# Optimization experiments

Hardware: AMD Instinct MI355X
Metric: run time of the kernel (lower is better)

Reference implementation:

```python
import jax, jax.numpy as jnp
import numpy as np

PRE_NMS = 4096
POST_NMS = 500
NMS_THRESH = 0.7


def setup_inputs() -> dict:
    key = jax.random.key(0)
    k1, k2, k3, k4, k5 = jax.random.split(key, 5)
    B, A = 4, 500000
    # anchors: [x, y, z, w, l, h, ry] with positive sizes, realistic ranges
    ctr = jax.random.uniform(k1, (B, A, 3)) * jnp.array([80.0, 80.0, 4.0])
    size = 1.0 + jax.random.uniform(k2, (B, A, 3)) * 3.0
    ry = (jax.random.uniform(k3, (B, A, 1)) - 0.5) * np.pi
    anchors = jnp.concatenate([ctr, size, ry], axis=-1)
    objectness = jax.random.normal(k4, (B, A))
    box_regression = jax.random.normal(k5, (B, A, 7)) * 0.1
    return {"anchors": anchors, "objectness": objectness, "box_regression": box_regression}


def decode(rel, anc):
    # SECOND-style 3D box decode (BoxCoder.decode)
    xa, ya, za = anc[..., 0], anc[..., 1], anc[..., 2]
    wa, la, ha = anc[..., 3], anc[..., 4], anc[..., 5]
    ra = anc[..., 6]
    diag = jnp.sqrt(wa * wa + la * la)
    xg = rel[..., 0] * diag + xa
    yg = rel[..., 1] * diag + ya
    zg = rel[..., 2] * ha + za
    wg = jnp.exp(rel[..., 3]) * wa
    lg = jnp.exp(rel[..., 4]) * la
    hg = jnp.exp(rel[..., 5]) * ha
    rg = rel[..., 6] + ra
    return jnp.stack([xg, yg, zg, wg, lg, hg, rg], axis=-1)


def bev_iou(b):
    # pairwise axis-aligned bird's-eye-view IoU; b: [K,7]
    x, y, w, l = b[:, 0], b[:, 1], b[:, 3], b[:, 4]
    x1, x2 = x - w * 0.5, x + w * 0.5
    y1, y2 = y - l * 0.5, y + l * 0.5
    iw = jnp.clip(jnp.minimum(x2[:, None], x2[None, :]) - jnp.maximum(x1[:, None], x1[None, :]), 0.0)
    ih = jnp.clip(jnp.minimum(y2[:, None], y2[None, :]) - jnp.maximum(y1[:, None], y1[None, :]), 0.0)
    inter = iw * ih
    area = w * l
    return inter / (area[:, None] + area[None, :] - inter + 1e-6)


def nms_keep(iou, thresh):
    # greedy NMS over score-sorted candidates; returns bool keep mask [K]
    K = iou.shape[0]
    idx = jnp.arange(K)

    def body(i, keep):
        sup = keep[i] & (iou[i] > thresh) & (idx > i)
        return keep & ~sup

    return jax.lax.fori_loop(0, K, body, jnp.ones((K,), dtype=bool))


def _per_image(anc, obj, reg):
    scores = jax.nn.sigmoid(obj)                    # [A]
    s_top, topk_idx = jax.lax.top_k(scores, PRE_NMS)  # sorted desc
    boxes = decode(reg[topk_idx], anc[topk_idx])      # [K,7]
    keep = nms_keep(bev_iou(boxes), NMS_THRESH)
    masked = jnp.where(keep, s_top, -1.0)
    _, sel = jax.lax.top_k(masked, POST_NMS)          # top post_nms kept boxes
    out_boxes = boxes[sel]                            # [P,7]
    out_scores = s_top[sel]                           # [P]
    return jnp.concatenate([out_boxes, out_scores[:, None]], axis=-1)  # [P,8]


def reference(anchors, objectness, box_regression):
    return jax.vmap(_per_image)(anchors, objectness, box_regression)  # [B,P,8]
```

## Files before the change

### kernel.cpp

```cpp
#include <hip/hip_runtime.h>
#include <hip/hip_bf16.h>

#define B_IMG 4
#define PRE_NMS 4096
#define POST_NMS 500
#define CAND_CAP 8192
#define BND_CAP 65536

typedef unsigned long long ull;

__device__ __forceinline__ unsigned key_of(float f) {
    unsigned u = __float_as_uint(f);
    return (u & 0x80000000u) ? ~u : (u | 0x80000000u);
}

__global__ void init_kernel(uint2* state, unsigned* hist, unsigned* count) {
    int t = blockIdx.x * blockDim.x + threadIdx.x;
    if (t < B_IMG) state[t] = make_uint2(0u, (unsigned)PRE_NMS);
    if (t < 2 * B_IMG) count[t] = 0u;
    if (t < B_IMG * 256) hist[t] = 0u;
}

__global__ void hist0_kernel(const float* __restrict__ obj, unsigned* __restrict__ hist, int A) {
    int b = blockIdx.y;
    __shared__ unsigned h[256];
    int t = threadIdx.x;
    int lane = t & 63;
    if (t < 256) h[t] = 0u;
    __syncthreads();
    const float* o = obj + (size_t)b * A;
    int stride = gridDim.x * blockDim.x;
    for (int i = blockIdx.x * blockDim.x + t;; i += stride) {
        bool valid = (i < A);
        ull vm = __ballot(valid);
        if (!vm) break;
        unsigned bin = valid ? (key_of(o[i]) >> 24) : 0xFFFFFFFFu;
        ull active = vm;
        while (active) {
            int leader = __ffsll((long long)active) - 1;
            unsigned lb = __shfl(bin, leader);
            ull m = __ballot(bin == lb) & active;
            if (lane == leader) atomicAdd(&h[lb], (unsigned)__popcll(m));
            active &= ~m;
        }
    }
    __syncthreads();
    if (t < 256 && h[t]) atomicAdd(&hist[b * 256 + t], h[t]);
}

__global__ void scan0_kernel(uint2* state, const unsigned* __restrict__ hist) {
    int b = threadIdx.x;
    if (b < B_IMG) {
        const unsigned* h = hist + b * 256;
        unsigned kneed = state[b].y;
        unsigned cum = 0;
        int d;
        for (d = 255; d > 0; d--) {
            unsigned c = h[d];
            if (cum + c >= kneed) break;
            cum += c;
        }
        state[b].x = (unsigned)d;
        state[b].y = kneed - cum;
    }
}

__global__ void compact_kernel(const float* __restrict__ obj, const uint2* __restrict__ state,
                               ull* __restrict__ bnd, unsigned* __restrict__ count, int A) {
    int b = blockIdx.y;
    unsigned d0 = state[b].x;
    __shared__ ull buf[2048];
    __shared__ unsigned lcnt, base;
    int t = threadIdx.x;
    if (t == 0) lcnt = 0u;
    __syncthreads();
    const float* o = obj + (size_t)b * A;
    int stride = gridDim.x * blockDim.x;
    for (int i = blockIdx.x * blockDim.x + t; i < A; i += stride) {
        unsigned key = key_of(o[i]);
        if ((key >> 24) >= d0) {
            unsigned p = atomicAdd(&lcnt, 1u);
            if (p < 2048u)
                buf[p] = ((ull)key << 32) | (unsigned)(0xFFFFFFFFu - (unsigned)i);
        }
    }
    __syncthreads();
    unsigned c = lcnt < 2048u ? lcnt : 2048u;
    if (t == 0) base = atomicAdd(&count[B_IMG + b], c);
    __syncthreads();
    for (unsigned p = t; p < c; p += blockDim.x) {
        unsigned pos = base + p;
        if (pos < BND_CAP) bnd[(size_t)b * BND_CAP + pos] = buf[p];
    }
}

__global__ void __launch_bounds__(1024) refine_kernel(const ull* __restrict__ bnd,
                                                      uint2* state,
                                                      ull* __restrict__ cand,
                                                      unsigned* __restrict__ count) {
    int b = blockIdx.x;
    __shared__ unsigned h[256];
    __shared__ unsigned sh_prefix, sh_kneed, sh_pos;
    int t = threadIdx.x;
    unsigned n = count[B_IMG + b];
    if (n > BND_CAP) n = BND_CAP;
    const ull* L = bnd + (size_t)b * BND_CAP;
    if (t == 0) { sh_prefix = state[b].x; sh_kneed = state[b].y; sh_pos = 0u; }
    for (int pass = 1; pass < 4; pass++) {
        if (t < 256) h[t] = 0u;
        __syncthreads();
        unsigned prefix = sh_prefix;
        int sh = 32 - 8 * pass;
        int dsh = 24 - 8 * pass;
        for (unsigned i = t; i < n; i += 1024) {
            unsigned key = (unsigned)(L[i] >> 32);
            if ((key >> sh) == prefix) atomicAdd(&h[(key >> dsh) & 255u], 1u);
        }
        __syncthreads();
        if (t == 0) {
            unsigned kneed = sh_kneed, cum = 0;
            int d;
            for (d = 255; d > 0; d--) {
                unsigned c = h[d];
                if (cum + c >= kneed) break;
                cum += c;
            }
            sh_prefix = (prefix << 8) | (unsigned)d;
            sh_kneed = kneed - cum;
        }
        __syncthreads();
    }
    unsigned T = sh_prefix;
    for (unsigned i = t; i < n; i += 1024) {
        ull v = L[i];
        if ((unsigned)(v >> 32) >= T) {
            unsigned p = atomicAdd(&sh_pos, 1u);
            if (p < CAND_CAP) cand[(size_t)b * CAND_CAP + p] = v;
        }
    }
    __syncthreads();
    if (t == 0) count[b] = sh_pos < CAND_CAP ? sh_pos : CAND_CAP;
}

__global__ void __launch_bounds__(256) rank_kernel(const ull* __restrict__ cand,
                                                   const unsigned* __restrict__ count,
                                                   unsigned* __restrict__ topk_idx,
                                                   const float* __restrict__ obj,
                                                   float* __restrict__ s_top, int A) {
    __shared__ ull s[CAND_CAP];
    int b = blockIdx.y;
    int t = threadIdx.x;
    unsigned cnt = count[b];
    if (cnt > CAND_CAP) cnt = CAND_CAP;
    const ull* C = cand + (size_t)b * CAND_CAP;
    unsigned cntR = (cnt + 7u) & ~7u;
    for (unsigned i = t; i < cntR; i += 256) s[i] = (i < cnt) ? C[i] : 0ull;
    __syncthreads();
    unsigned c = blockIdx.x * 256 + t;
    if (c >= cnt) return;
    ull me = s[c];
    unsigned rank = 0;
#pragma unroll 1
    for (unsigned j = 0; j < cntR; j += 8) {
        rank += (unsigned)(s[j]     > me) + (unsigned)(s[j + 1] > me)
              + (unsigned)(s[j + 2] > me) + (unsigned)(s[j + 3] > me)
              + (unsigned)(s[j + 4] > me) + (unsigned)(s[j + 5] > me)
              + (unsigned)(s[j + 6] > me) + (unsigned)(s[j + 7] > me);
    }
    if (rank < PRE_NMS) {
        unsigned idx = 0xFFFFFFFFu - (unsigned)(me & 0xFFFFFFFFull);
        topk_idx[b * PRE_NMS + rank] = idx;
        float x = obj[(size_t)b * A + idx];
        s_top[b * PRE_NMS + rank] = 1.0f / (1.0f + expf(-x));
    }
}

__global__ void decode_kernel(const float* __restrict__ anchors, const float* __restrict__ reg,
                              const unsigned* __restrict__ topk_idx, float* __restrict__ boxes,
                              float* __restrict__ X1, float* __restrict__ X2,
                              float* __restrict__ Y1, float* __restrict__ Y2,
                              float* __restrict__ AREA, int A) {
    int b = blockIdx.y;
    int r = blockIdx.x * 256 + threadIdx.x;
    if (r >= PRE_NMS) return;
    unsigned idx = topk_idx[b * PRE_NMS + r];
    const float* an = anchors + ((size_t)b * A + idx) * 7;
    const float* rg = reg + ((size_t)b * A + idx) * 7;
    float xa = an[0], ya = an[1], za = an[2], wa = an[3], la = an[4], ha = an[5], ra = an[6];
    float diag = sqrtf(wa * wa + la * la);
    float xg = rg[0] * diag + xa;
    float yg = rg[1] * diag + ya;
    float zg = rg[2] * ha + za;
    float wg = expf(rg[3]) * wa;
    float lg = expf(rg[4]) * la;
    float hg = expf(rg[5]) * ha;
    float rr = rg[6] + ra;
    float* o = boxes + ((size_t)b * PRE_NMS + r) * 7;
    o[0] = xg; o[1] = yg; o[2] = zg; o[3] = wg; o[4] = lg; o[5] = hg; o[6] = rr;
    int q = b * PRE_NMS + r;
    X1[q] = xg - wg * 0.5f;
    X2[q] = xg + wg * 0.5f;
    Y1[q] = yg - lg * 0.5f;
    Y2[q] = yg + lg * 0.5f;
    AREA[q] = wg * lg;
}

__global__ void mask_kernel(const float* __restrict__ X1, const float* __restrict__ X2,
                            const float* __restrict__ Y1, const float* __restrict__ Y2,
                            const float* __restrict__ AREA, ull* __restrict__ mask) {
    int b = blockIdx.y;
    int t = blockIdx.x * 256 + threadIdx.x;
    int i = t & (PRE_NMS - 1);
    int w = t >> 12;
    int q0 = b * PRE_NMS;
    float x1i = X1[q0 + i], x2i = X2[q0 + i];
    float y1i = Y1[q0 + i], y2i = Y2[q0 + i];
    float ai = AREA[q0 + i];
    ull word = 0ull;
    int jbase = w << 6;
#pragma unroll 4
    for (int k = 0; k < 64; k++) {
        int j = jbase + k;
        float iw = fminf(x2i, X2[q0 + j]) - fmaxf(x1i, X1[q0 + j]);
        iw = fmaxf(iw, 0.0f);
        float ih = fminf(y2i, Y2[q0 + j]) - fmaxf(y1i, Y1[q0 + j]);
        ih = fmaxf(ih, 0.0f);
        float inter = iw * ih;
        float den = ai + AREA[q0 + j] - inter + 1e-6f;
        float iou = inter / den;
        word |= ((ull)((iou > 0.7f) && (j > i))) << k;
    }
    mask[((size_t)b * PRE_NMS + i) * 64 + w] = word;
}

#define LOAD_TILE(BUF, WT) do {                                               \
    const ull* _base = Mb + ((size_t)(WT) << 12) + lane;                      \
    _Pragma("unroll")                                                         \
    for (int _k = 0; _k < 64; _k++) BUF[_k] = _base[(size_t)_k << 6];         \
} while (0)

#define LOAD_D(DST, WT) (DST) = Mb[((size_t)(WT) << 12) + ((size_t)lane << 6) + (WT)]

#define PROCESS(W, CURB, DCUR, NXTB, DNXT) do {                               \
    ull cur = __shfl(K, (W));                                                 \
    if ((W) + 1 < 64) { LOAD_D(DNXT, (W) + 1); LOAD_TILE(NXTB, (W) + 1); }    \
    ull active = __ballot((DCUR) != 0ull) & cur;                              \
    while (active) {                                                          \
        int _kk = __ffsll((long long)active) - 1;                             \
        ull dk = __shfl((DCUR), _kk);                                         \
        cur &= ~dk; active &= ~dk; active &= ~(1ull << _kk);                  \
    }                                                                         \
    ull sup = 0ull;                                                           \
    _Pragma("unroll")                                                         \
    for (int _k = 0; _k < 64; _k++)                                           \
        sup |= ((cur >> _k) & 1ull) ? CURB[_k] : 0ull;                        \
    K &= ~sup;                                                                \
} while (0)

__global__ void __launch_bounds__(64, 1) nms_kernel(const ull* __restrict__ mask,
                                                    ull* __restrict__ keep_out) {
    int b = blockIdx.x;
    int lane = threadIdx.x;
    const ull* Mb = mask + (size_t)b * PRE_NMS * 64;
    ull K = ~0ull;
    ull bufA[64], bufB[64];
    ull da = 0ull, db = 0ull;
    LOAD_D(da, 0);
    LOAD_TILE(bufA, 0);
    for (int w = 0; w < 64; w += 2) {
        PROCESS(w, bufA, da, bufB, db);
        PROCESS(w + 1, bufB, db, bufA, da);
    }
    keep_out[b * 64 + lane] = K;
}

__global__ void select_write_kernel(const ull* __restrict__ keep,
                                    const float* __restrict__ boxes,
                                    const float* __restrict__ s_top,
                                    float* __restrict__ out) {
    int b = blockIdx.x;
    __shared__ int cnts[64];
    __shared__ int bases[65];
    __shared__ int sel[POST_NMS];
    int t = threadIdx.x;
    if (t < 64) cnts[t] = __popcll(keep[b * 64 + t]);
    __syncthreads();
    if (t == 0) {
        int acc = 0;
        for (int w = 0; w < 64; w++) { bases[w] = acc; acc += cnts[w]; }
        bases[64] = acc;
    }
    __syncthreads();
    if (t < 64) {
        ull kw = keep[b * 64 + t];
        int K_total = bases[64];
        int kr = bases[t];
        int ur = t * 64 - bases[t];
        for (int k = 0; k < 64; k++) {
            int i = t * 64 + k;
            if ((kw >> k) & 1ull) {
                if (kr < POST_NMS) sel[kr] = i;
                kr++;
            } else {
                int pos = K_total + ur;
                if (pos < POST_NMS) sel[pos] = i;
                ur++;
            }
        }
    }
    __syncthreads();
    for (int r = t; r < POST_NMS; r += 512) {
        int i = sel[r];
        const float* bx = boxes + ((size_t)b * PRE_NMS + i) * 7;
        float* o = out + ((size_t)b * POST_NMS + r) * 8;
#pragma unroll
        for (int c = 0; c < 7; c++) o[c] = bx[c];
        o[7] = s_top[b * PRE_NMS + i];
    }
}

extern "C" void kernel_launch(void* const* d_in, const int* in_sizes, int n_in,
                              void* d_out, int out_size, void* d_ws, size_t ws_size,
                              hipStream_t stream) {
    const float* anchors = (const float*)d_in[0];
    const float* obj = (const float*)d_in[1];
    const float* reg = (const float*)d_in[2];
    float* out = (float*)d_out;
    const int A = in_sizes[1] / B_IMG;

    auto align = [](size_t x) { return (x + 255) & ~(size_t)255; };
    char* p = (char*)d_ws;
    uint2* state = (uint2*)p;     p += align(B_IMG * sizeof(uint2));
    unsigned* hist = (unsigned*)p; p += align(B_IMG * 256 * sizeof(unsigned));
    unsigned* count = (unsigned*)p; p += align(2 * B_IMG * sizeof(unsigned));
    ull* cand = (ull*)p;          p += align((size_t)B_IMG * CAND_CAP * 8);
    ull* bnd = (ull*)p;           p += align((size_t)B_IMG * BND_CAP * 8);
    unsigned* topk = (unsigned*)p; p += align((size_t)B_IMG * PRE_NMS * 4);
    float* s_top = (float*)p;     p += align((size_t)B_IMG * PRE_NMS * 4);
    float* boxes = (float*)p;     p += align((size_t)B_IMG * PRE_NMS * 7 * 4);
    float* X1 = (float*)p;        p += align((size_t)B_IMG * PRE_NMS * 4);
    float* X2 = (float*)p;        p += align((size_t)B_IMG * PRE_NMS * 4);
    float* Y1 = (float*)p;        p += align((size_t)B_IMG * PRE_NMS * 4);
    float* Y2 = (float*)p;        p += align((size_t)B_IMG * PRE_NMS * 4);
    float* AREA = (float*)p;      p += align((size_t)B_IMG * PRE_NMS * 4);
    ull* mask = (ull*)p;          p += align((size_t)B_IMG * PRE_NMS * 64 * 8);
    ull* keep = (ull*)p;          p += align((size_t)B_IMG * 64 * 8);

    init_kernel<<<4, 256, 0, stream>>>(state, hist, count);
    hist0_kernel<<<dim3(256, B_IMG), 256, 0, stream>>>(obj, hist, A);
    scan0_kernel<<<1, 64, 0, stream>>>(state, hist);
    compact_kernel<<<dim3(256, B_IMG), 256, 0, stream>>>(obj, state, bnd, count, A);
    refine_kernel<<<B_IMG, 1024, 0, stream>>>(bnd, state, cand, count);
    rank_kernel<<<dim3(CAND_CAP / 256, B_IMG), 256, 0, stream>>>(cand, count, topk, obj, s_top, A);
    decode_kernel<<<dim3(PRE_NMS / 256, B_IMG), 256, 0, stream>>>(anchors, reg, topk, boxes,
                                                                  X1, X2, Y1, Y2, AREA, A);
    mask_kernel<<<dim3(PRE_NMS * 64 / 256, B_IMG), 256, 0, stream>>>(X1, X2, Y1, Y2, AREA, mask);
    nms_kernel<<<B_IMG, 64, 0, stream>>>(mask, keep);
    select_write_kernel<<<B_IMG, 512, 0, stream>>>(keep, boxes, s_top, out);
}
```

Before: 390.8 us.

## Fuse rank/decode and NMS/select kernels, vectorize histogram and compaction

Replaces the ballot-based histogram with float4 loads into four replicated shared histograms and writes per-block partial histograms, so the init kernel and global atomics go away. The scan kernel now also resets the counters. Compaction reads float4. Rank and decode are fused into one kernel that reads candidates straight from global memory and recovers the score from the key. The mask kernel writes zeros for tiles whose mask can only be zero, the NMS scan is spread across 4 wavefronts with shared-memory reductions, and it is fused with the select/write step. Together these cut launches and memory traffic, at the cost of more barriers inside the NMS loop.

Result: slower. 460.3 us (+17.8%).

```diff
diff --git a/kernel.cpp b/kernel.cpp
--- a/kernel.cpp
+++ b/kernel.cpp
@@ -6,6 +6,7 @@
 #define POST_NMS 500
 #define CAND_CAP 8192
 #define BND_CAP 65536
+#define HBLK 256
 
 typedef unsigned long long ull;
 
@@ -14,54 +15,52 @@
     return (u & 0x80000000u) ? ~u : (u | 0x80000000u);
 }
 
-__global__ void init_kernel(uint2* state, unsigned* hist, unsigned* count) {
-    int t = blockIdx.x * blockDim.x + threadIdx.x;
-    if (t < B_IMG) state[t] = make_uint2(0u, (unsigned)PRE_NMS);
-    if (t < 2 * B_IMG) count[t] = 0u;
-    if (t < B_IMG * 256) hist[t] = 0u;
-}
-
-__global__ void hist0_kernel(const float* __restrict__ obj, unsigned* __restrict__ hist, int A) {
+__global__ void hist0_kernel(const float* __restrict__ obj, unsigned* __restrict__ histPart, int A) {
     int b = blockIdx.y;
+    __shared__ unsigned h[4][256];
+    int t = threadIdx.x;
+#pragma unroll
+    for (int r = 0; r < 4; r++) h[r][t] = 0u;
+    __syncthreads();
+    const float4* o4 = (const float4*)(obj + (size_t)b * A);
+    int n4 = A >> 2;
+    int stride = gridDim.x * blockDim.x;
+    int rep = t & 3;
+    for (int i = blockIdx.x * blockDim.x + t; i < n4; i += stride) {
+        float4 v = o4[i];
+        atomicAdd(&h[rep][key_of(v.x) >> 24], 1u);
+        atomicAdd(&h[rep][key_of(v.y) >> 24], 1u);
+        atomicAdd(&h[rep][key_of(v.z) >> 24], 1u);
+        atomicAdd(&h[rep][key_of(v.w) >> 24], 1u);
+    }
+    if (blockIdx.x == 0 && t < (A & 3)) {
+        unsigned k = key_of(obj[(size_t)b * A + (A & ~3) + t]);
+        atomicAdd(&h[rep][k >> 24], 1u);
+    }
+    __syncthreads();
+    histPart[((size_t)b * HBLK + blockIdx.x) * 256 + t] = h[0][t] + h[1][t] + h[2][t] + h[3][t];
+}
+
+__global__ void scan0_kernel(uint2* state, const unsigned* __restrict__ histPart,
+                             unsigned* __restrict__ count) {
+    int b = blockIdx.x;
+    int t = threadIdx.x;
     __shared__ unsigned h[256];
-    int t = threadIdx.x;
-    int lane = t & 63;
-    if (t < 256) h[t] = 0u;
-    __syncthreads();
-    const float* o = obj + (size_t)b * A;
-    int stride = gridDim.x * blockDim.x;
-    for (int i = blockIdx.x * blockDim.x + t;; i += stride) {
-        bool valid = (i < A);
-        ull vm = __ballot(valid);
-        if (!vm) break;
-        unsigned bin = valid ? (key_of(o[i]) >> 24) : 0xFFFFFFFFu;
-        ull active = vm;
-        while (active) {
-            int leader = __ffsll((long long)active) - 1;
-            unsigned lb = __shfl(bin, leader);
-            ull m = __ballot(bin == lb) & active;
-            if (lane == leader) atomicAdd(&h[lb], (unsigned)__popcll(m));
-            active &= ~m;
-        }
-    }
-    __syncthreads();
-    if (t < 256 && h[t]) atomicAdd(&hist[b * 256 + t], h[t]);
-}
-
-__global__ void scan0_kernel(uint2* state, const unsigned* __restrict__ hist) {
-    int b = threadIdx.x;
-    if (b < B_IMG) {
-        const unsigned* h = hist + b * 256;
-        unsigned kneed = state[b].y;
-        unsigned cum = 0;
+    unsigned s = 0;
+    for (int blk = 0; blk < HBLK; blk++) s += histPart[((size_t)b * HBLK + blk) * 256 + t];
+    h[t] = s;
+    __syncthreads();
+    if (t == 0) {
+        unsigned kneed = PRE_NMS, cum = 0;
         int d;
         for (d = 255; d > 0; d--) {
             unsigned c = h[d];
             if (cum + c >= kneed) break;
             cum += c;
         }
-        state[b].x = (unsigned)d;
-        state[b].y = kneed - cum;
+        state[b] = make_uint2((unsigned)d, kneed - cum);
+        count[b] = 0u;
+        count[B_IMG + b] = 0u;
     }
 }
 
@@ -74,15 +73,22 @@
     int t = threadIdx.x;
     if (t == 0) lcnt = 0u;
     __syncthreads();
-    const float* o = obj + (size_t)b * A;
+    const float4* o4 = (const float4*)(obj + (size_t)b * A);
+    int n4 = A >> 2;
     int stride = gridDim.x * blockDim.x;
-    for (int i = blockIdx.x * blockDim.x + t; i < A; i += stride) {
-        unsigned key = key_of(o[i]);
-        if ((key >> 24) >= d0) {
-            unsigned p = atomicAdd(&lcnt, 1u);
-            if (p < 2048u)
-                buf[p] = ((ull)key << 32) | (unsigned)(0xFFFFFFFFu - (unsigned)i);
-        }
+    for (int i = blockIdx.x * blockDim.x + t; i < n4; i += stride) {
+        float4 v = o4[i];
+        unsigned i0 = (unsigned)i * 4u;
+        unsigned k0 = key_of(v.x), k1 = key_of(v.y), k2 = key_of(v.z), k3 = key_of(v.w);
+        if ((k0 >> 24) >= d0) { unsigned p = atomicAdd(&lcnt, 1u); if (p < 2048u) buf[p] = ((ull)k0 << 32) | (0xFFFFFFFFu - i0); }
+        if ((k1 >> 24) >= d0) { unsigned p = atomicAdd(&lcnt, 1u); if (p < 2048u) buf[p] = ((ull)k1 << 32) | (0xFFFFFFFFu - (i0 + 1u)); }
+        if ((k2 >> 24) >= d0) { unsigned p = atomicAdd(&lcnt, 1u); if (p < 2048u) buf[p] = ((ull)k2 << 32) | (0xFFFFFFFFu - (i0 + 2u)); }
+        if ((k3 >> 24) >= d0) { unsigned p = atomicAdd(&lcnt, 1u); if (p < 2048u) buf[p] = ((ull)k3 << 32) | (0xFFFFFFFFu - (i0 + 3u)); }
+    }
+    if (blockIdx.x == 0 && t < (A & 3)) {
+        unsigned ii = (unsigned)(A & ~3) + t;
+        unsigned k = key_of(obj[(size_t)b * A + ii]);
+        if ((k >> 24) >= d0) { unsigned p = atomicAdd(&lcnt, 1u); if (p < 2048u) buf[p] = ((ull)k << 32) | (0xFFFFFFFFu - ii); }
     }
     __syncthreads();
     unsigned c = lcnt < 2048u ? lcnt : 2048u;
@@ -95,7 +101,7 @@
 }
 
 __global__ void __launch_bounds__(1024) refine_kernel(const ull* __restrict__ bnd,
-                                                      uint2* state,
+                                                      const uint2* __restrict__ state,
                                                       ull* __restrict__ cand,
                                                       unsigned* __restrict__ count) {
     int b = blockIdx.x;
@@ -110,8 +116,7 @@
         if (t < 256) h[t] = 0u;
         __syncthreads();
         unsigned prefix = sh_prefix;
-        int sh = 32 - 8 * pass;
-        int dsh = 24 - 8 * pass;
+        int sh = 32 - 8 * pass, dsh = 24 - 8 * pass;
         for (unsigned i = t; i < n; i += 1024) {
             unsigned key = (unsigned)(L[i] >> 32);
             if ((key >> sh) == prefix) atomicAdd(&h[(key >> dsh) & 255u], 1u);
@@ -135,69 +140,58 @@
         ull v = L[i];
         if ((unsigned)(v >> 32) >= T) {
             unsigned p = atomicAdd(&sh_pos, 1u);
-            if (p < CAND_CAP) cand[(size_t)b * CAND_CAP + p] = v;
-        }
-    }
-    __syncthreads();
-    if (t == 0) count[b] = sh_pos < CAND_CAP ? sh_pos : CAND_CAP;
-}
-
-__global__ void __launch_bounds__(256) rank_kernel(const ull* __restrict__ cand,
-                                                   const unsigned* __restrict__ count,
-                                                   unsigned* __restrict__ topk_idx,
-                                                   const float* __restrict__ obj,
-                                                   float* __restrict__ s_top, int A) {
-    __shared__ ull s[CAND_CAP];
+            if (p < CAND_CAP) cand[(size_t)b * (CAND_CAP + 8) + p] = v;
+        }
+    }
+    __syncthreads();
+    if (t < 8) {
+        unsigned cc = sh_pos < CAND_CAP ? sh_pos : CAND_CAP;
+        cand[(size_t)b * (CAND_CAP + 8) + cc + t] = 0ull;
+        if (t == 0) count[b] = cc;
+    }
+}
+
+__global__ void __launch_bounds__(256) rankdecode_kernel(
+        const ull* __restrict__ cand, const unsigned* __restrict__ count,
+        const float* __restrict__ anchors, const float* __restrict__ reg,
+        float* __restrict__ boxes, float* __restrict__ X1, float* __restrict__ X2,
+        float* __restrict__ Y1, float* __restrict__ Y2, float* __restrict__ AREA,
+        float* __restrict__ s_top, int A) {
     int b = blockIdx.y;
-    int t = threadIdx.x;
     unsigned cnt = count[b];
     if (cnt > CAND_CAP) cnt = CAND_CAP;
-    const ull* C = cand + (size_t)b * CAND_CAP;
+    unsigned c = blockIdx.x * 256 + threadIdx.x;
+    if (c >= cnt) return;
+    const ull* C = cand + (size_t)b * (CAND_CAP + 8);
+    ull me = C[c];
     unsigned cntR = (cnt + 7u) & ~7u;
-    for (unsigned i = t; i < cntR; i += 256) s[i] = (i < cnt) ? C[i] : 0ull;
-    __syncthreads();
-    unsigned c = blockIdx.x * 256 + t;
-    if (c >= cnt) return;
-    ull me = s[c];
     unsigned rank = 0;
-#pragma unroll 1
     for (unsigned j = 0; j < cntR; j += 8) {
-        rank += (unsigned)(s[j]     > me) + (unsigned)(s[j + 1] > me)
-              + (unsigned)(s[j + 2] > me) + (unsigned)(s[j + 3] > me)
-              + (unsigned)(s[j + 4] > me) + (unsigned)(s[j + 5] > me)
-              + (unsigned)(s[j + 6] > me) + (unsigned)(s[j + 7] > me);
-    }
-    if (rank < PRE_NMS) {
-        unsigned idx = 0xFFFFFFFFu - (unsigned)(me & 0xFFFFFFFFull);
-        topk_idx[b * PRE_NMS + rank] = idx;
-        float x = obj[(size_t)b * A + idx];
-        s_top[b * PRE_NMS + rank] = 1.0f / (1.0f + expf(-x));
-    }
-}
-
-__global__ void decode_kernel(const float* __restrict__ anchors, const float* __restrict__ reg,
-                              const unsigned* __restrict__ topk_idx, float* __restrict__ boxes,
-                              float* __restrict__ X1, float* __restrict__ X2,
-                              float* __restrict__ Y1, float* __restrict__ Y2,
-                              float* __restrict__ AREA, int A) {
-    int b = blockIdx.y;
-    int r = blockIdx.x * 256 + threadIdx.x;
-    if (r >= PRE_NMS) return;
-    unsigned idx = topk_idx[b * PRE_NMS + r];
+        rank += (unsigned)(C[j]     > me) + (unsigned)(C[j + 1] > me)
+              + (unsigned)(C[j + 2] > me) + (unsigned)(C[j + 3] > me)
+              + (unsigned)(C[j + 4] > me) + (unsigned)(C[j + 5] > me)
+              + (unsigned)(C[j + 6] > me) + (unsigned)(C[j + 7] > me);
+    }
+    if (rank >= PRE_NMS) return;
+    unsigned key = (unsigned)(me >> 32);
+    unsigned idx = 0xFFFFFFFFu - (unsigned)(me & 0xFFFFFFFFull);
+    unsigned ub = (key & 0x80000000u) ? (key & 0x7FFFFFFFu) : ~key;
+    float x = __uint_as_float(ub);
+    s_top[b * PRE_NMS + rank] = 1.0f / (1.0f + expf(-x));
     const float* an = anchors + ((size_t)b * A + idx) * 7;
     const float* rg = reg + ((size_t)b * A + idx) * 7;
     float xa = an[0], ya = an[1], za = an[2], wa = an[3], la = an[4], ha = an[5], ra = an[6];
-    float diag = sqrtf(wa * wa + la * la);
-    float xg = rg[0] * diag + xa;
-    float yg = rg[1] * diag + ya;
+    float diagv = sqrtf(wa * wa + la * la);
+    float xg = rg[0] * diagv + xa;
+    float yg = rg[1] * diagv + ya;
     float zg = rg[2] * ha + za;
     float wg = expf(rg[3]) * wa;
     float lg = expf(rg[4]) * la;
     float hg = expf(rg[5]) * ha;
     float rr = rg[6] + ra;
-    float* o = boxes + ((size_t)b * PRE_NMS + r) * 7;
+    float* o = boxes + ((size_t)b * PRE_NMS + rank) * 7;
     o[0] = xg; o[1] = yg; o[2] = zg; o[3] = wg; o[4] = lg; o[5] = hg; o[6] = rr;
-    int q = b * PRE_NMS + r;
+    int q = b * PRE_NMS + rank;
     X1[q] = xg - wg * 0.5f;
     X2[q] = xg + wg * 0.5f;
     Y1[q] = yg - lg * 0.5f;
@@ -212,6 +206,8 @@
     int t = blockIdx.x * 256 + threadIdx.x;
     int i = t & (PRE_NMS - 1);
     int w = t >> 12;
+    size_t mi = ((size_t)b * PRE_NMS + i) * 64 + w;
+    if (i >= ((w + 1) << 6)) { mask[mi] = 0ull; return; }
     int q0 = b * PRE_NMS;
     float x1i = X1[q0 + i], x2i = X2[q0 + i];
     float y1i = Y1[q0 + i], y2i = Y2[q0 + i];
@@ -230,60 +226,75 @@
         float iou = inter / den;
         word |= ((ull)((iou > 0.7f) && (j > i))) << k;
     }
-    mask[((size_t)b * PRE_NMS + i) * 64 + w] = word;
-}
-
-#define LOAD_TILE(BUF, WT) do {                                               \
-    const ull* _base = Mb + ((size_t)(WT) << 12) + lane;                      \
-    _Pragma("unroll")                                                         \
-    for (int _k = 0; _k < 64; _k++) BUF[_k] = _base[(size_t)_k << 6];         \
-} while (0)
-
-#define LOAD_D(DST, WT) (DST) = Mb[((size_t)(WT) << 12) + ((size_t)lane << 6) + (WT)]
-
-#define PROCESS(W, CURB, DCUR, NXTB, DNXT) do {                               \
-    ull cur = __shfl(K, (W));                                                 \
-    if ((W) + 1 < 64) { LOAD_D(DNXT, (W) + 1); LOAD_TILE(NXTB, (W) + 1); }    \
-    ull active = __ballot((DCUR) != 0ull) & cur;                              \
-    while (active) {                                                          \
-        int _kk = __ffsll((long long)active) - 1;                             \
-        ull dk = __shfl((DCUR), _kk);                                         \
-        cur &= ~dk; active &= ~dk; active &= ~(1ull << _kk);                  \
-    }                                                                         \
-    ull sup = 0ull;                                                           \
-    _Pragma("unroll")                                                         \
-    for (int _k = 0; _k < 64; _k++)                                           \
-        sup |= ((cur >> _k) & 1ull) ? CURB[_k] : 0ull;                        \
-    K &= ~sup;                                                                \
-} while (0)
-
-__global__ void __launch_bounds__(64, 1) nms_kernel(const ull* __restrict__ mask,
-                                                    ull* __restrict__ keep_out) {
+    mask[mi] = word;
+}
+
+__global__ void __launch_bounds__(256, 1) nms_select_kernel(
+        const ull* __restrict__ mask, const float* __restrict__ boxes,
+        const float* __restrict__ s_top, float* __restrict__ out) {
     int b = blockIdx.x;
-    int lane = threadIdx.x;
+    int t = threadIdx.x;
+    int lane = t & 63, v = t >> 6;
+    int rbase = v * 16;
     const ull* Mb = mask + (size_t)b * PRE_NMS * 64;
-    ull K = ~0ull;
-    ull bufA[64], bufB[64];
-    ull da = 0ull, db = 0ull;
-    LOAD_D(da, 0);
-    LOAD_TILE(bufA, 0);
-    for (int w = 0; w < 64; w += 2) {
-        PROCESS(w, bufA, da, bufB, db);
-        PROCESS(w + 1, bufB, db, bufA, da);
-    }
-    keep_out[b * 64 + lane] = K;
-}
-
-__global__ void select_write_kernel(const ull* __restrict__ keep,
-                                    const float* __restrict__ boxes,
-                                    const float* __restrict__ s_top,
-                                    float* __restrict__ out) {
-    int b = blockIdx.x;
+    __shared__ ull diag[2][64];
+    __shared__ ull part[2][4][64];
+    __shared__ ull keepw[64];
     __shared__ int cnts[64];
     __shared__ int bases[65];
     __shared__ int sel[POST_NMS];
-    int t = threadIdx.x;
-    if (t < 64) cnts[t] = __popcll(keep[b * 64 + t]);
+    ull K = ~0ull;
+    ull b0[16], b1[16], b2[16], b3[16];
+
+#define PREF(W, BUF) do {                                                          \
+    _Pragma("unroll")                                                              \
+    for (int kk = 0; kk < 16; kk++)                                                \
+        BUF[kk] = Mb[(((size_t)(W) * 64 + rbase + kk) << 6) + lane];               \
+} while (0)
+
+#define TILE(W, BUF) do {                                                          \
+    int par = (W) & 1;                                                             \
+    ull cur = __shfl(K, (W));                                                      \
+    if (lane == (W)) {                                                             \
+        _Pragma("unroll")                                                          \
+        for (int kk = 0; kk < 16; kk++) diag[par][rbase + kk] = BUF[kk];           \
+    }                                                                              \
+    __syncthreads();                                                               \
+    ull dl = diag[par][lane];                                                      \
+    ull active = __ballot(dl != 0ull) & cur;                                       \
+    while (active) {                                                               \
+        int kk = __ffsll((long long)active) - 1;                                   \
+        ull dk = __shfl(dl, kk);                                                   \
+        cur &= ~dk; active &= ~dk; active &= ~(1ull << kk);                        \
+    }                                                                              \
+    ull sup = 0ull;                                                                \
+    _Pragma("unroll")                                                              \
+    for (int kk = 0; kk < 16; kk++)                                                \
+        sup |= ((cur >> (rbase + kk)) & 1ull) ? BUF[kk] : 0ull;                    \
+    part[par][v][lane] = sup;                                                      \
+    __syncthreads();                                                               \
+    K &= ~(part[par][0][lane] | part[par][1][lane] |                               \
+           part[par][2][lane] | part[par][3][lane]);                               \
+    if ((W) + 4 < 64) {                                                            \
+        _Pragma("unroll")                                                          \
+        for (int kk = 0; kk < 16; kk++)                                            \
+            BUF[kk] = Mb[((((size_t)(W) + 4) * 64 + rbase + kk) << 6) + lane];     \
+    }                                                                              \
+} while (0)
+
+    PREF(0, b0); PREF(1, b1); PREF(2, b2); PREF(3, b3);
+    for (int w = 0; w < 64; w += 4) {
+        TILE(w + 0, b0);
+        TILE(w + 1, b1);
+        TILE(w + 2, b2);
+        TILE(w + 3, b3);
+    }
+#undef PREF
+#undef TILE
+
+    if (v == 0) keepw[lane] = K;
+    __syncthreads();
+    if (t < 64) cnts[t] = __popcll(keepw[t]);
     __syncthreads();
     if (t == 0) {
         int acc = 0;
@@ -292,7 +303,7 @@
     }
     __syncthreads();
     if (t < 64) {
-        ull kw = keep[b * 64 + t];
+        ull kw = keepw[t];
         int K_total = bases[64];
         int kr = bases[t];
         int ur = t * 64 - bases[t];
@@ -309,7 +320,7 @@
         }
     }
     __syncthreads();
-    for (int r = t; r < POST_NMS; r += 512) {
+    for (int r = t; r < POST_NMS; r += 256) {
         int i = sel[r];
         const float* bx = boxes + ((size_t)b * PRE_NMS + i) * 7;
         float* o = out + ((size_t)b * POST_NMS + r) * 8;
@@ -330,31 +341,26 @@
 
     auto align = [](size_t x) { return (x + 255) & ~(size_t)255; };
     char* p = (char*)d_ws;
-    uint2* state = (uint2*)p;     p += align(B_IMG * sizeof(uint2));
-    unsigned* hist = (unsigned*)p; p += align(B_IMG * 256 * sizeof(unsigned));
+    uint2* state = (uint2*)p;       p += align(B_IMG * sizeof(uint2));
+    unsigned* histPart = (unsigned*)p; p += align((size_t)B_IMG * HBLK * 256 * 4);
     unsigned* count = (unsigned*)p; p += align(2 * B_IMG * sizeof(unsigned));
-    ull* cand = (ull*)p;          p += align((size_t)B_IMG * CAND_CAP * 8);
-    ull* bnd = (ull*)p;           p += align((size_t)B_IMG * BND_CAP * 8);
-    unsigned* topk = (unsigned*)p; p += align((size_t)B_IMG * PRE_NMS * 4);
-    float* s_top = (float*)p;     p += align((size_t)B_IMG * PRE_NMS * 4);
-    float* boxes = (float*)p;     p += align((size_t)B_IMG * PRE_NMS * 7 * 4);
-    float* X1 = (float*)p;        p += align((size_t)B_IMG * PRE_NMS * 4);
-    float* X2 = (float*)p;        p += align((size_t)B_IMG * PRE_NMS * 4);
-    float* Y1 = (float*)p;        p += align((size_t)B_IMG * PRE_NMS * 4);
-    float* Y2 = (float*)p;        p += align((size_t)B_IMG * PRE_NMS * 4);
-    float* AREA = (float*)p;      p += align((size_t)B_IMG * PRE_NMS * 4);
-    ull* mask = (ull*)p;          p += align((size_t)B_IMG * PRE_NMS * 64 * 8);
-    ull* keep = (ull*)p;          p += align((size_t)B_IMG * 64 * 8);
-
-    init_kernel<<<4, 256, 0, stream>>>(state, hist, count);
-    hist0_kernel<<<dim3(256, B_IMG), 256, 0, stream>>>(obj, hist, A);
-    scan0_kernel<<<1, 64, 0, stream>>>(state, hist);
-    compact_kernel<<<dim3(256, B_IMG), 256, 0, stream>>>(obj, state, bnd, count, A);
+    ull* cand = (ull*)p;            p += align((size_t)B_IMG * (CAND_CAP + 8) * 8);
+    ull* bnd = (ull*)p;             p += align((size_t)B_IMG * BND_CAP * 8);
+    float* s_top = (float*)p;       p += align((size_t)B_IMG * PRE_NMS * 4);
+    float* boxes = (float*)p;       p += align((size_t)B_IMG * PRE_NMS * 7 * 4);
+    float* X1 = (float*)p;          p += align((size_t)B_IMG * PRE_NMS * 4);
+    float* X2 = (float*)p;          p += align((size_t)B_IMG * PRE_NMS * 4);
+    float* Y1 = (float*)p;          p += align((size_t)B_IMG * PRE_NMS * 4);
+    float* Y2 = (float*)p;          p += align((size_t)B_IMG * PRE_NMS * 4);
+    float* AREA = (float*)p;        p += align((size_t)B_IMG * PRE_NMS * 4);
+    ull* mask = (ull*)p;            p += align((size_t)B_IMG * PRE_NMS * 64 * 8);
+
+    hist0_kernel<<<dim3(HBLK, B_IMG), 256, 0, stream>>>(obj, histPart, A);
+    scan0_kernel<<<B_IMG, 256, 0, stream>>>(state, histPart, count);
+    compact_kernel<<<dim3(HBLK, B_IMG), 256, 0, stream>>>(obj, state, bnd, count, A);
     refine_kernel<<<B_IMG, 1024, 0, stream>>>(bnd, state, cand, count);
-    rank_kernel<<<dim3(CAND_CAP / 256, B_IMG), 256, 0, stream>>>(cand, count, topk, obj, s_top, A);
-    decode_kernel<<<dim3(PRE_NMS / 256, B_IMG), 256, 0, stream>>>(anchors, reg, topk, boxes,
-                                                                  X1, X2, Y1, Y2, AREA, A);
+    rankdecode_kernel<<<dim3(CAND_CAP / 256, B_IMG), 256, 0, stream>>>(
+        cand, count, anchors, reg, boxes, X1, X2, Y1, Y2, AREA, s_top, A);
     mask_kernel<<<dim3(PRE_NMS * 64 / 256, B_IMG), 256, 0, stream>>>(X1, X2, Y1, Y2, AREA, mask);
-    nms_kernel<<<B_IMG, 64, 0, stream>>>(mask, keep);
-    select_write_kernel<<<B_IMG, 512, 0, stream>>>(keep, boxes, s_top, out);
-}
+    nms_select_kernel<<<B_IMG, 256, 0, stream>>>(mask, boxes, s_top, out);
+}
```
